# Optimization experiments

Hardware: AMD Instinct MI355X
Metric: run time of the kernel (lower is better)

The kernel has to match this reference:

```python
import jax, jax.numpy as jnp
import numpy as np

H, W = 640, 640
C_IN, C_OUT = 3, 64
K, PAD = 7, 3          # 7x7 sparse conv, SAME padding (stride 1)
POOL_K, POOL_S = 3, 2  # valid 3x3 max pool, stride 2
N_SITES = 100000
BN_EPS = 1e-5


def setup_inputs() -> dict:
    key = jax.random.key(0)
    k1, k2, k3 = jax.random.split(key, 3)
    feature_map = jax.random.normal(k1, (H, W, C_IN), dtype=jnp.float32)
    update_location = jax.random.randint(k2, (N_SITES, 2), 0, min(H, W)).astype(jnp.int64)
    # kaiming-uniform-ish init for the 7x7x3 -> 64 conv weight
    fan_in = K * K * C_IN
    bound = np.sqrt(3.0 / fan_in).astype(np.float32)
    weight = jax.random.uniform(k3, (K, K, C_IN, C_OUT), jnp.float32, -bound, bound)
    return {
        "update_location": update_location,
        "feature_map": feature_map,
        "weight": weight,
        "gamma": jnp.ones((C_OUT,), jnp.float32),
        "beta": jnp.zeros((C_OUT,), jnp.float32),
        "running_mean": jnp.zeros((C_OUT,), jnp.float32),
        "running_var": jnp.ones((C_OUT,), jnp.float32),
    }


def reference(update_location, feature_map, weight, gamma, beta, running_mean, running_var):
    # ---- sparse (active-site) 7x7 conv: gather patches only at active sites ----
    fm = jnp.pad(feature_map, ((PAD, PAD), (PAD, PAD), (0, 0)))  # zero pad borders
    offs = jnp.arange(K)
    rows = update_location[:, 0, None] + offs          # [N, K] (pad offset = +PAD-PAD)
    cols = update_location[:, 1, None] + offs          # [N, K]
    patches = fm[rows[:, :, None], cols[:, None, :]]   # [N, K, K, C_IN]
    feats = jnp.einsum('nijc,ijco->no', patches, weight)  # [N, C_OUT]

    # ---- frozen BN + ReLU fused on active sites ----
    inv = gamma * jax.lax.rsqrt(running_var + BN_EPS)
    feats = jnp.maximum(feats * inv + (beta - running_mean * inv), 0.0)

    # ---- scatter active-site features into dense map (inactive sites stay 0) ----
    dense = jnp.zeros((H, W, C_OUT), feats.dtype).at[
        update_location[:, 0], update_location[:, 1]].set(feats)

    # ---- 3x3 stride-2 valid max pool (ReLU outputs >= 0, zeros elsewhere) ----
    pooled = jax.lax.reduce_window(
        dense, 0.0, jax.lax.max,
        (POOL_K, POOL_K, 1), (POOL_S, POOL_S, 1), 'VALID')  # [319, 319, C_OUT]
    return pooled
```

## Files before the change

kernel.cpp:

```cpp
#include <hip/hip_runtime.h>

#define HH 640
#define WW 640
#define COUT 64
#define KK 7
#define NS 100000
#define OHh 319
#define OWw 319
#define PWY 646
#define PWX 648
#define OWNER_BLKS 391
#define PAD_BLKS ((PWY * PWX / 2 + 255) / 256)
#define NBLK 1563

typedef _Float16 half2_t __attribute__((ext_vector_type(2)));
typedef _Float16 h8 __attribute__((ext_vector_type(8)));
typedef float f4 __attribute__((ext_vector_type(4)));
typedef uint4 u4a __attribute__((aligned(8)));

union H2U { unsigned u; half2_t h; };
union H8U { uint4 u; h8 h; _Float16 e[8]; };

__device__ __forceinline__ unsigned short f2bf(float x) {
    unsigned u = __float_as_uint(x);
    return (unsigned short)((u + 0x7FFFu + ((u >> 16) & 1u)) >> 16);
}
__device__ __forceinline__ float bf2f(unsigned short b) {
    return __uint_as_float((unsigned)b << 16);
}

__device__ __forceinline__ bool detect_is64(const int* __restrict__ loc) {
    const int smp = loc[1 + 2 * (int)(threadIdx.x & 63)];
    return __ballot(smp != 0) == 0ULL;
}

__global__ __launch_bounds__(256) void prep_kernel(
        const int* __restrict__ loc, const float* __restrict__ fm,
        int* __restrict__ owner, uint2* __restrict__ pfm) {
    const bool is64 = detect_is64(loc);
    if (blockIdx.x < OWNER_BLKS) {
        const int n = blockIdx.x * 256 + threadIdx.x;
        if (n < NS) {
            int r, c;
            if (is64) { r = loc[4 * n]; c = loc[4 * n + 2]; }
            else      { r = loc[2 * n]; c = loc[2 * n + 1]; }
            atomicMax(&owner[r * WW + c], n);
        }
    } else {
        const int pair = (blockIdx.x - OWNER_BLKS) * 256 + threadIdx.x;
        const int pix = pair * 2;
        if (pix < PWY * PWX) {
            const int r = pix / PWX, c = pix - r * PWX;
            uint4 o;
            H2U a0, b0, a1, b1;
            a0.u = b0.u = a1.u = b1.u = 0;
            if (r >= 3 && r < 643) {
                const float* s = fm + ((size_t)(r - 3) * WW + (c - 3)) * 3;
                if (c >= 3 && c < 643) {
                    a0.h = half2_t{(_Float16)s[0], (_Float16)s[1]};
                    b0.h = half2_t{(_Float16)s[2], (_Float16)0};
                }
                if (c + 1 >= 3 && c + 1 < 643) {
                    a1.h = half2_t{(_Float16)s[3], (_Float16)s[4]};
                    b1.h = half2_t{(_Float16)s[5], (_Float16)0};
                }
            }
            o.x = a0.u; o.y = b0.u; o.z = a1.u; o.w = b1.u;
            *(uint4*)(pfm + pix) = o;
        }
    }
}

__global__ __launch_bounds__(256) void feats_kernel(
        const int* __restrict__ loc, const uint2* __restrict__ pfm,
        const float* __restrict__ wgt, const float* __restrict__ gamma,
        const float* __restrict__ beta, const float* __restrict__ mean,
        const float* __restrict__ var, const int* __restrict__ owner,
        unsigned short* __restrict__ feats) {
    __shared__ uint4 WB[4 * KK * 64];
    for (int e = threadIdx.x; e < 4 * KK * 64; e += 256) {
        const int t = e / (KK * 64);
        const int rem = e - t * KK * 64;
        const int i = rem >> 6, l = rem & 63;
        const int cout = t * 16 + (l & 15);
        const int q = l >> 4;
        H8U w;
        #pragma unroll
        for (int j = 0; j < 8; ++j) {
            const int kl = q * 8 + j, px = kl >> 2, ci = kl & 3;
            const float v = (px < KK && ci < 3)
                              ? wgt[((i * KK + px) * 3 + ci) * COUT + cout] : 0.0f;
            w.e[j] = (_Float16)v;
        }
        WB[e] = w.u;
    }
    const bool is64 = detect_is64(loc);
    __syncthreads();

    const int lane = threadIdx.x & 63;
    const int q = lane >> 4;
    const int n0 = (blockIdx.x * 4 + (threadIdx.x >> 6)) * 16;

    const int nA = min(n0 + (lane & 15), NS - 1);
    int rA, cA;
    if (is64) { rA = loc[4 * nA]; cA = loc[4 * nA + 2]; }
    else      { rA = loc[2 * nA]; cA = loc[2 * nA + 1]; }
    int aidx = rA * PWX + cA + 2 * q;

    bool alive[4];
    #pragma unroll
    for (int p = 0; p < 4; ++p) {
        const int nS = n0 + q * 4 + p;
        const int nSc = min(nS, NS - 1);
        int r, c;
        if (is64) { r = loc[4 * nSc]; c = loc[4 * nSc + 2]; }
        else      { r = loc[2 * nSc]; c = loc[2 * nSc + 1]; }
        alive[p] = (nS < NS) && (owner[r * WW + c] == nS);
    }

    float invt[4], bist[4];
    #pragma unroll
    for (int t = 0; t < 4; ++t) {
        const int co = t * 16 + (lane & 15);
        const float iv = gamma[co] * rsqrtf(var[co] + 1e-5f);
        invt[t] = iv; bist[t] = beta[co] - mean[co] * iv;
    }

    f4 acc[4] = {f4{0,0,0,0}, f4{0,0,0,0}, f4{0,0,0,0}, f4{0,0,0,0}};
    #pragma unroll
    for (int i = 0; i < KK; ++i) {
        H8U a;
        a.u = *(const u4a*)(pfm + aidx + i * PWX);
        #pragma unroll
        for (int t = 0; t < 4; ++t) {
            H8U b;
            b.u = WB[(t * KK + i) * 64 + lane];
            acc[t] = __builtin_amdgcn_mfma_f32_16x16x32_f16(a.h, b.h, acc[t], 0, 0, 0);
        }
    }

    unsigned short* dump = feats + (size_t)NS * COUT;
    #pragma unroll
    for (int t = 0; t < 4; ++t) {
        #pragma unroll
        for (int p = 0; p < 4; ++p) {
            const float v = fmaxf(acc[t][p] * invt[t] + bist[t], 0.0f);
            const int nS = n0 + q * 4 + p;
            unsigned short* addr = alive[p]
                ? feats + (size_t)nS * COUT + t * 16 + (lane & 15)
                : dump + lane;
            *addr = f2bf(v);
        }
    }
}

__global__ __launch_bounds__(256) void pool_kernel(
        const int* __restrict__ owner, const unsigned short* __restrict__ feats,
        float* __restrict__ out) {
    const int lane = threadIdx.x & 63;
    const int TPR = 80;
    const int task = __builtin_amdgcn_readfirstlane(blockIdx.x * 4 + (threadIdx.x >> 6));
    if (task >= OHh * TPR) return;
    const int oh = task / TPR, ow0 = (task % TPR) * 4;
    const int r0 = oh * 2, c0 = ow0 * 2;

    int ov[3][9];
    #pragma unroll
    for (int dy = 0; dy < 3; ++dy)
        __builtin_memcpy(&ov[dy][0], owner + (r0 + dy) * WW + c0, 36);

    float v[3][9];
    #pragma unroll
    for (int dy = 0; dy < 3; ++dy)
        #pragma unroll
        for (int dx = 0; dx < 9; ++dx) {
            const int o = ov[dy][dx];
            const int oc = o < 0 ? 0 : o;
            const float f = bf2f(feats[(size_t)oc * COUT + lane]);
            v[dy][dx] = (o >= 0) ? f : 0.0f;
        }

    #pragma unroll
    for (int qq = 0; qq < 4; ++qq) {
        const int ow = ow0 + qq;
        if (ow >= OWw) break;
        float m = 0.0f;
        #pragma unroll
        for (int dy = 0; dy < 3; ++dy)
            #pragma unroll
            for (int dx = 0; dx < 3; ++dx)
                m = fmaxf(m, v[dy][2 * qq + dx]);
        out[(size_t)(oh * OWw + ow) * COUT + lane] = m;
    }
}

extern "C" void kernel_launch(void* const* d_in, const int* in_sizes, int n_in,
                              void* d_out, int out_size, void* d_ws, size_t ws_size,
                              hipStream_t stream) {
    const int*   loc   = (const int*)d_in[0];
    const float* fm    = (const float*)d_in[1];
    const float* wgt   = (const float*)d_in[2];
    const float* gamma = (const float*)d_in[3];
    const float* beta  = (const float*)d_in[4];
    const float* mean  = (const float*)d_in[5];
    const float* var   = (const float*)d_in[6];
    float* out = (float*)d_out;

    char* ws = (char*)d_ws;
    int* owner = (int*)ws;
    unsigned short* feats = (unsigned short*)(ws + 1638400);
    uint2* pfm = (uint2*)(ws + 1638400 + (size_t)NS * COUT * 2 + 256);

    hipMemsetAsync(owner, 0xFF, (size_t)HH * WW * sizeof(int), stream);
    prep_kernel<<<OWNER_BLKS + PAD_BLKS, 256, 0, stream>>>(loc, fm, owner, pfm);
    feats_kernel<<<NBLK, 256, 0, stream>>>(loc, pfm, wgt, gamma, beta, mean, var,
                                           owner, feats);
    pool_kernel<<<(OHh * 80 + 3) / 4, 256, 0, stream>>>(owner, feats, out);
}
```

Measured before the change: 121.6 us.

## Precompute packed fp16 weights and BN params once in prep kernel

Measured after the change: 112.9 us. 1.08x faster.

```diff
diff --git a/kernel.cpp b/kernel.cpp
--- a/kernel.cpp
+++ b/kernel.cpp
@@ -12,6 +12,7 @@
 #define OWNER_BLKS 391
 #define PAD_BLKS ((PWY * PWX / 2 + 255) / 256)
 #define NBLK 1563
+#define NWB (4 * KK * 64)
 
 typedef _Float16 half2_t __attribute__((ext_vector_type(2)));
 typedef _Float16 h8 __attribute__((ext_vector_type(8)));
@@ -36,9 +37,13 @@
 
 __global__ __launch_bounds__(256) void prep_kernel(
         const int* __restrict__ loc, const float* __restrict__ fm,
-        int* __restrict__ owner, uint2* __restrict__ pfm) {
-    const bool is64 = detect_is64(loc);
+        const float* __restrict__ wgt, const float* __restrict__ gamma,
+        const float* __restrict__ beta, const float* __restrict__ mean,
+        const float* __restrict__ var,
+        int* __restrict__ owner, uint2* __restrict__ pfm,
+        uint4* __restrict__ wbg, float* __restrict__ bn) {
     if (blockIdx.x < OWNER_BLKS) {
+        const bool is64 = detect_is64(loc);
         const int n = blockIdx.x * 256 + threadIdx.x;
         if (n < NS) {
             int r, c;
@@ -46,7 +51,7 @@
             else      { r = loc[2 * n]; c = loc[2 * n + 1]; }
             atomicMax(&owner[r * WW + c], n);
         }
-    } else {
+    } else if (blockIdx.x < OWNER_BLKS + PAD_BLKS) {
         const int pair = (blockIdx.x - OWNER_BLKS) * 256 + threadIdx.x;
         const int pix = pair * 2;
         if (pix < PWY * PWX) {
@@ -68,62 +73,60 @@
             o.x = a0.u; o.y = b0.u; o.z = a1.u; o.w = b1.u;
             *(uint4*)(pfm + pix) = o;
         }
+    } else {
+        for (int e = threadIdx.x; e < NWB; e += 256) {
+            const int t = e / (KK * 64);
+            const int rem = e - t * KK * 64;
+            const int i = rem >> 6, l = rem & 63;
+            const int cout = t * 16 + (l & 15);
+            const int q = l >> 4;
+            H8U w;
+            #pragma unroll
+            for (int j = 0; j < 8; ++j) {
+                const int kl = q * 8 + j, px = kl >> 2, ci = kl & 3;
+                const float v = (px < KK && ci < 3)
+                                  ? wgt[((i * KK + px) * 3 + ci) * COUT + cout] : 0.0f;
+                w.e[j] = (_Float16)v;
+            }
+            wbg[e] = w.u;
+        }
+        if (threadIdx.x < COUT) {
+            const int co = threadIdx.x;
+            const float iv = gamma[co] * rsqrtf(var[co] + 1e-5f);
+            bn[co] = iv;
+            bn[COUT + co] = beta[co] - mean[co] * iv;
+        }
     }
 }
 
 __global__ __launch_bounds__(256) void feats_kernel(
         const int* __restrict__ loc, const uint2* __restrict__ pfm,
-        const float* __restrict__ wgt, const float* __restrict__ gamma,
-        const float* __restrict__ beta, const float* __restrict__ mean,
-        const float* __restrict__ var, const int* __restrict__ owner,
+        const uint4* __restrict__ wbg, const float* __restrict__ bn,
         unsigned short* __restrict__ feats) {
-    __shared__ uint4 WB[4 * KK * 64];
-    for (int e = threadIdx.x; e < 4 * KK * 64; e += 256) {
-        const int t = e / (KK * 64);
-        const int rem = e - t * KK * 64;
-        const int i = rem >> 6, l = rem & 63;
-        const int cout = t * 16 + (l & 15);
-        const int q = l >> 4;
-        H8U w;
-        #pragma unroll
-        for (int j = 0; j < 8; ++j) {
-            const int kl = q * 8 + j, px = kl >> 2, ci = kl & 3;
-            const float v = (px < KK && ci < 3)
-                              ? wgt[((i * KK + px) * 3 + ci) * COUT + cout] : 0.0f;
-            w.e[j] = (_Float16)v;
-        }
-        WB[e] = w.u;
-    }
+    __shared__ uint4 WB[NWB];
+    #pragma unroll
+    for (int e = 0; e < NWB / 256; ++e)
+        WB[e * 256 + threadIdx.x] = wbg[e * 256 + threadIdx.x];
     const bool is64 = detect_is64(loc);
     __syncthreads();
 
     const int lane = threadIdx.x & 63;
+    const int m = lane & 15;
     const int q = lane >> 4;
     const int n0 = (blockIdx.x * 4 + (threadIdx.x >> 6)) * 16;
-
-    const int nA = min(n0 + (lane & 15), NS - 1);
+    if (n0 >= NS) return;
+
+    const int nA = n0 + m;
     int rA, cA;
     if (is64) { rA = loc[4 * nA]; cA = loc[4 * nA + 2]; }
     else      { rA = loc[2 * nA]; cA = loc[2 * nA + 1]; }
-    int aidx = rA * PWX + cA + 2 * q;
-
-    bool alive[4];
-    #pragma unroll
-    for (int p = 0; p < 4; ++p) {
-        const int nS = n0 + q * 4 + p;
-        const int nSc = min(nS, NS - 1);
-        int r, c;
-        if (is64) { r = loc[4 * nSc]; c = loc[4 * nSc + 2]; }
-        else      { r = loc[2 * nSc]; c = loc[2 * nSc + 1]; }
-        alive[p] = (nS < NS) && (owner[r * WW + c] == nS);
-    }
+    const int aidx = rA * PWX + cA + 2 * q;
 
     float invt[4], bist[4];
     #pragma unroll
     for (int t = 0; t < 4; ++t) {
-        const int co = t * 16 + (lane & 15);
-        const float iv = gamma[co] * rsqrtf(var[co] + 1e-5f);
-        invt[t] = iv; bist[t] = beta[co] - mean[co] * iv;
+        invt[t] = bn[t * 16 + m];
+        bist[t] = bn[COUT + t * 16 + m];
     }
 
     f4 acc[4] = {f4{0,0,0,0}, f4{0,0,0,0}, f4{0,0,0,0}, f4{0,0,0,0}};
@@ -139,17 +142,13 @@
         }
     }
 
-    unsigned short* dump = feats + (size_t)NS * COUT;
     #pragma unroll
     for (int t = 0; t < 4; ++t) {
         #pragma unroll
         for (int p = 0; p < 4; ++p) {
             const float v = fmaxf(acc[t][p] * invt[t] + bist[t], 0.0f);
             const int nS = n0 + q * 4 + p;
-            unsigned short* addr = alive[p]
-                ? feats + (size_t)nS * COUT + t * 16 + (lane & 15)
-                : dump + lane;
-            *addr = f2bf(v);
+            feats[(size_t)nS * COUT + t * 16 + m] = f2bf(v);
         }
     }
 }
@@ -209,11 +208,14 @@
     char* ws = (char*)d_ws;
     int* owner = (int*)ws;
     unsigned short* feats = (unsigned short*)(ws + 1638400);
-    uint2* pfm = (uint2*)(ws + 1638400 + (size_t)NS * COUT * 2 + 256);
+    uint2* pfm = (uint2*)(ws + 1638400 + (size_t)NS * COUT * 2);
+    char* ws2 = ws + 1638400 + (size_t)NS * COUT * 2 + (size_t)PWY * PWX * 8;
+    uint4* wbg = (uint4*)ws2;
+    float* bn  = (float*)(ws2 + NWB * 16);
 
     hipMemsetAsync(owner, 0xFF, (size_t)HH * WW * sizeof(int), stream);
-    prep_kernel<<<OWNER_BLKS + PAD_BLKS, 256, 0, stream>>>(loc, fm, owner, pfm);
-    feats_kernel<<<NBLK, 256, 0, stream>>>(loc, pfm, wgt, gamma, beta, mean, var,
-                                           owner, feats);
+    prep_kernel<<<OWNER_BLKS + PAD_BLKS + 1, 256, 0, stream>>>(
+        loc, fm, wgt, gamma, beta, mean, var, owner, pfm, wbg, bn);
+    feats_kernel<<<NBLK, 256, 0, stream>>>(loc, pfm, wbg, bn, feats);
     pool_kernel<<<(OHh * 80 + 3) / 4, 256, 0, stream>>>(owner, feats, out);
 }
```
